# Kernel optimization log

Hardware: AMD Instinct MI355X
Metric: run time of the kernel (lower is better)

Reference implementation:

```python
import jax, jax.numpy as jnp
import numpy as np

TARGET_RADIUS = 0.95
EPS = 1e-8

def _spectral_norm_wh(W_h, u):
    # Power iteration (3 steps) is done under no_grad in the original torch code,
    # so u, v are constants w.r.t. differentiation.
    Ws = jax.lax.stop_gradient(W_h)
    v = None
    for _ in range(3):
        v = Ws.T @ u
        v = v / (jnp.linalg.norm(v) + EPS)
        u = Ws @ v
        u = u / (jnp.linalg.norm(u) + EPS)
    sigma = jnp.abs(u @ W_h @ v)  # gradient flows through W_h here
    return W_h * (TARGET_RADIUS / (sigma + EPS))


def setup_inputs() -> dict:
    key = jax.random.key(0)
    kx, kwx, kwh, ku = jax.random.split(key, 4)
    T, B, D = 2048, 8, 1024
    x = jax.random.normal(kx, (T, B, D), dtype=jnp.float32)
    h0 = jnp.zeros((B, D), dtype=jnp.float32)
    W_x = jax.random.normal(kwx, (D, D), dtype=jnp.float32) * 0.02
    W_h = jax.random.normal(kwh, (D, D), dtype=jnp.float32) * (1.0 / np.sqrt(D))
    b = jnp.zeros((D,), dtype=jnp.float32)
    u = jax.random.normal(ku, (D,), dtype=jnp.float32)
    u = u / jnp.linalg.norm(u)
    return {"x": x, "h0": h0, "W_x": W_x, "W_h": W_h, "b": b, "u": u}


def reference(x, h0, W_x, W_h, b, u):
    # x: [T, B, D], h0: [B, D]
    Wh = _spectral_norm_wh(W_h, u)
    # Input projection is independent of the recurrence: one big GEMM.
    pre = jnp.einsum('tbd,ed->tbe', x, W_x) + b  # [T, B, D]

    def step(h_prev, p_t):
        h_new = p_t + h_prev @ Wh.T  # linear recurrence, no tanh
        return h_new, h_new

    _, hs = jax.lax.scan(step, h0, pre)  # hs: [T, B, D]
    h_all = jnp.concatenate([h0[None], hs], axis=0)  # [T+1, B, D]
    output = hs * (hs * jax.nn.sigmoid(hs))  # h * silu(h)
    return output, h_all
```

## Files before the change

### kernel.cpp

```cpp
#include <hip/hip_runtime.h>
#include <hip/hip_bf16.h>

#define DEV __device__ __forceinline__

typedef __bf16 bf16x8 __attribute__((ext_vector_type(8)));
typedef float  f32x4  __attribute__((ext_vector_type(4)));
typedef unsigned short u16;

DEV u16   f2b(float f) { __bf16 h = (__bf16)f; return __builtin_bit_cast(u16, h); }
DEV float b2f(u16 x)   { return __builtin_bit_cast(float, ((unsigned)x) << 16); }

DEV void gl_lds16(const u16* g, u16* l) {
  __builtin_amdgcn_global_load_lds((const __attribute__((address_space(1))) void*)g,
                                   (__attribute__((address_space(3))) void*)l, 16, 0, 0);
}

DEV long arow(int m, int S, int j) {
  if (S > 0)  return ((long)((m >> 3) * S + j)) * 8 + (m & 7);
  if (S == 0) return m;
  return m & 7;
}

struct ZCfg {
  const u16 *A0, *A1, *A2, *A3, *A4;
  const u16 *B0, *B1, *B2, *B3, *B4;
  int S0, J0, S1, J1, S2, J2, S3, J3, S4, J4;
  int nseg, mvalid, q;
  const float* addc;
  const float* addf; int addS, addJ;
  const u16* addb; int abJ;
  float* outf;
  u16 *outb, *outbT, *outlo;
  u16* outm; int oS, oJ;
  float *hall, *out0;
};
struct GArgs { ZCfg z0, z1, z2, z3; };

template<int MODE>
__global__ __launch_bounds__(256) void gU(GArgs ga)
{
  ZCfg c;
  switch (blockIdx.z) { case 0: c = ga.z0; break; case 1: c = ga.z1; break;
                        case 2: c = ga.z2; break; default: c = ga.z3; break; }
  const int K = c.nseg << 10;

  int tid = threadIdx.x, lane = tid & 63, w = tid >> 6;
  int wrow = (w >> 1) << 5, wcol = (w & 1) << 5;
  int m0 = blockIdx.y << 6, e0 = blockIdx.x << 6;

  __shared__ u16 As[2][8192], Bs[2][8192];
  f32x4 acc[2][2] = {};

  int rA[4], cA[4];
#pragma unroll
  for (int j = 0; j < 4; ++j) {
    int p = (j * 4 + w) * 1024 + lane * 16;
    int r = p >> 8, o = (p & 255) ^ ((r & 7) << 4);
    rA[j] = r; cA[j] = o >> 1;
  }
  auto seg = [&](int i, const u16*& A, int& S, int& J, const u16*& B) {
    switch (i) {
      case 0: A = c.A0; S = c.S0; J = c.J0; B = c.B0; break;
      case 1: A = c.A1; S = c.S1; J = c.J1; B = c.B1; break;
      case 2: A = c.A2; S = c.S2; J = c.J2; B = c.B2; break;
      case 3: A = c.A3; S = c.S3; J = c.J3; B = c.B3; break;
      default: A = c.A4; S = c.S4; J = c.J4; B = c.B4; break;
    }
  };
  auto stage = [&](int buf, int kt) {
    int si = kt >> 10, kl = kt & 1023;
    const u16 *A, *B; int S, J;
    seg(si, A, S, J, B);
#pragma unroll
    for (int j = 0; j < 4; ++j) {
      int grow = m0 + rA[j];
      gl_lds16(A + arow(grow, S, J) * 1024 + kl + cA[j], &As[buf][(j * 4 + w) * 512]);
    }
#pragma unroll
    for (int j = 0; j < 4; ++j)
      gl_lds16(B + (size_t)(e0 + rA[j]) * 1024 + kl + cA[j], &Bs[buf][(j * 4 + w) * 512]);
  };

  stage(0, 0);
  asm volatile("s_waitcnt vmcnt(0)" ::: "memory");
  __syncthreads();

  int buf = 0;
  for (int kt = 0; kt < K; kt += 128, buf ^= 1) {
    if (kt + 128 < K) stage(buf ^ 1, kt + 128);
#pragma unroll
    for (int ks = 0; ks < 4; ++ks) {
      int oa = ks * 64 + ((lane >> 4) << 4);
      bf16x8 af[2], bf[2];
#pragma unroll
      for (int s = 0; s < 2; ++s) {
        int ra = wrow + s * 16 + (lane & 15);
        int rb = wcol + s * 16 + (lane & 15);
        af[s] = *(const bf16x8*)((const char*)&As[buf][0] + ra * 256 + (oa ^ ((ra & 7) << 4)));
        bf[s] = *(const bf16x8*)((const char*)&Bs[buf][0] + rb * 256 + (oa ^ ((rb & 7) << 4)));
      }
#pragma unroll
      for (int ms = 0; ms < 2; ++ms)
#pragma unroll
        for (int ns = 0; ns < 2; ++ns)
          acc[ms][ns] = __builtin_amdgcn_mfma_f32_16x16x32_bf16(af[ms], bf[ns], acc[ms][ns], 0, 0, 0);
    }
    asm volatile("s_waitcnt vmcnt(0)" ::: "memory");
    __syncthreads();
  }

  int l4 = ((lane >> 4) << 2), lc = lane & 15;
#pragma unroll
  for (int ms = 0; ms < 2; ++ms)
#pragma unroll
    for (int ns = 0; ns < 2; ++ns)
#pragma unroll
      for (int j = 0; j < 4; ++j) {
        int row = m0 + wrow + ms * 16 + l4 + j;
        int col = e0 + wcol + ns * 16 + lc;
        float v = acc[ms][ns][j];
        if (MODE == 0) {
          u16 h = f2b(v);
          if (c.outb)  c.outb[(size_t)row * 1024 + col] = h;
          if (c.outbT) c.outbT[(size_t)col * 1024 + row] = h;
        } else if (MODE == 1) {
          v += c.addc[col];
          c.outf[(size_t)row * 1024 + col] = v;
          c.outb[(size_t)row * 1024 + col] = f2b(v);
        } else if (MODE == 2) {
          if (c.addf) v += c.addf[arow(row, c.addS, c.addJ) * 1024 + col];
          if (row < c.mvalid) {
            if (c.outf) c.outf[(size_t)row * 1024 + col] = v;
            u16 hi = f2b(v);
            if (c.outb)  c.outb[(size_t)row * 1024 + col] = hi;
            if (c.outlo) c.outlo[(size_t)row * 1024 + col] = f2b(v - b2f(hi));
            if (c.outm)  c.outm[arow(row, c.oS, c.oJ) * 1024 + col] = hi;
          }
        } else {
          v += b2f(c.addb[arow(row, 4, c.abJ) * 1024 + col]);
          int t = (row >> 3) * 4 + c.q, b = row & 7;
          c.hall[(size_t)t * 8192 + b * 1024 + col] = v;
          float sg = 1.f / (1.f + __expf(-v));
          c.out0[(size_t)(t - 1) * 8192 + b * 1024 + col] = v * v * sg;
          if (c.outb) c.outb[(size_t)row * 1024 + col] = f2b(v);
        }
      }
}

__global__ void k_init(const float* __restrict__ u_in, const float* __restrict__ h0,
                       float* __restrict__ u_cur, float* __restrict__ v_acc,
                       float* __restrict__ u_acc, float* __restrict__ hall0)
{
  int i = blockIdx.x * 256 + threadIdx.x;
  if (i < 1024) { u_cur[i] = u_in[i]; v_acc[i] = 0.f; u_acc[i] = 0.f; }
  if (i < 8192) hall0[i] = h0[i];
}

__global__ void k_bnd0(const float* __restrict__ h0, float* __restrict__ bndS,
                       u16* __restrict__ bndSb, u16* __restrict__ bndSlo,
                       u16* __restrict__ bndb)
{
  int i = blockIdx.x * 256 + threadIdx.x;
  float h = h0[i];
  bndS[i] = h;
  u16 hi = f2b(h);
  bndSb[i] = hi;
  bndSlo[i] = f2b(h - b2f(hi));
  bndb[i] = hi;
}

__global__ void k_v(const float* __restrict__ W, const float* __restrict__ u_cur,
                    float* __restrict__ v_acc)
{
  int d = blockIdx.x * 256 + threadIdx.x;
  int e0 = blockIdx.y * 64;
  float a = 0.f;
  for (int e = e0; e < e0 + 64; ++e) a += W[(size_t)e * 1024 + d] * u_cur[e];
  atomicAdd(&v_acc[d], a);
}

__global__ void k_u(const float* __restrict__ W, const float* __restrict__ v_cur,
                    float* __restrict__ u_acc)
{
  int lg = threadIdx.x & 15, ei = threadIdx.x >> 4;
  int e = blockIdx.y * 16 + ei;
  int d0 = blockIdx.x * 512;
  float a = 0.f;
  for (int i = 0; i < 32; ++i) { int d = d0 + lg + 16 * i; a += W[(size_t)e * 1024 + d] * v_cur[d]; }
#pragma unroll
  for (int m = 1; m < 16; m <<= 1) a += __shfl_xor(a, m);
  if (lg == 0) atomicAdd(&u_acc[e], a);
}

__global__ void k_norm(const float* __restrict__ acc, float* __restrict__ outv,
                       float* __restrict__ z1)
{
  __shared__ float red[16];
  int t = threadIdx.x;
  float x = acc[t];
  float ss = x * x;
#pragma unroll
  for (int m = 1; m < 64; m <<= 1) ss += __shfl_xor(ss, m);
  if ((t & 63) == 0) red[t >> 6] = ss;
  __syncthreads();
  if (t < 64) {
    float s = (t < 16) ? red[t] : 0.f;
#pragma unroll
    for (int m = 1; m < 16; m <<= 1) s += __shfl_xor(s, m);
    if (t == 0) red[0] = s;
  }
  __syncthreads();
  float nrm = sqrtf(red[0]) + 1e-8f;
  outv[t] = x / nrm;
  z1[t] = 0.f;
}

__global__ void k_sigma(const float* __restrict__ acc, float* __restrict__ scale)
{
  __shared__ float red[16];
  int t = threadIdx.x;
  float x = acc[t];
  float ss = x * x;
#pragma unroll
  for (int m = 1; m < 64; m <<= 1) ss += __shfl_xor(ss, m);
  if ((t & 63) == 0) red[t >> 6] = ss;
  __syncthreads();
  if (t < 64) {
    float s = (t < 16) ? red[t] : 0.f;
#pragma unroll
    for (int m = 1; m < 16; m <<= 1) s += __shfl_xor(s, m);
    if (t == 0) {
      float sigma = s / (sqrtf(s) + 1e-8f);
      scale[0] = 0.95f / (sigma + 1e-8f);
    }
  }
}

__global__ void k_prep(const float* __restrict__ Wh, const float* __restrict__ Wx,
                       const float* __restrict__ scale, u16* __restrict__ wh_b,
                       u16* __restrict__ whT, u16* __restrict__ wxb)
{
  int i = blockIdx.x * 256 + threadIdx.x;
  float s = scale[0];
  int e = i >> 10, d = i & 1023;
  u16 hw = f2b(Wh[i] * s);
  wh_b[i] = hw;
  whT[(size_t)d * 1024 + e] = hw;
  wxb[i] = f2b(Wx[i]);
}

__global__ void k_cvt(const float* __restrict__ in, u16* __restrict__ out, int n)
{
  int i = (blockIdx.x * 256 + threadIdx.x) * 4;
  if (i >= n) return;
  float4 v = *(const float4*)(in + i);
  ushort4 o;
  o.x = f2b(v.x); o.y = f2b(v.y); o.z = f2b(v.z); o.w = f2b(v.w);
  *(ushort4*)(out + i) = o;
}

__global__ void k_gather(const float* __restrict__ lC, u16* __restrict__ lamH,
                         u16* __restrict__ lamL)
{
  int i = blockIdx.x * 256 + threadIdx.x;
  int r = i >> 8, e4 = (i & 255) * 4;
  int src = (r >> 3) * 128 + (r & 7);
  float4 v = *(const float4*)(lC + (size_t)src * 1024 + e4);
  ushort4 hi, lo;
  hi.x = f2b(v.x); lo.x = f2b(v.x - b2f(hi.x));
  hi.y = f2b(v.y); lo.y = f2b(v.y - b2f(hi.y));
  hi.z = f2b(v.z); lo.z = f2b(v.z - b2f(hi.z));
  hi.w = f2b(v.w); lo.w = f2b(v.w - b2f(hi.w));
  *(ushort4*)(lamH + (size_t)r * 1024 + e4) = hi;
  *(ushort4*)(lamL + (size_t)r * 1024 + e4) = lo;
}

static void setseg(ZCfg& z, int i, const u16* A, int S, int J, const u16* B) {
  switch (i) {
    case 0: z.A0 = A; z.S0 = S; z.J0 = J; z.B0 = B; break;
    case 1: z.A1 = A; z.S1 = S; z.J1 = J; z.B1 = B; break;
    case 2: z.A2 = A; z.S2 = S; z.J2 = J; z.B2 = B; break;
    case 3: z.A3 = A; z.S3 = S; z.J3 = J; z.B3 = B; break;
    default: z.A4 = A; z.S4 = S; z.J4 = J; z.B4 = B; break;
  }
}

extern "C" void kernel_launch(void* const* d_in, const int* in_sizes, int n_in,
                              void* d_out, int out_size, void* d_ws, size_t ws_size,
                              hipStream_t stream)
{
  (void)in_sizes; (void)n_in; (void)out_size; (void)ws_size;
  const float* x  = (const float*)d_in[0];
  const float* h0 = (const float*)d_in[1];
  const float* Wx = (const float*)d_in[2];
  const float* Wh = (const float*)d_in[3];
  const float* bv = (const float*)d_in[4];
  const float* uv = (const float*)d_in[5];

  float* out0 = (float*)d_out;
  float* hall = out0 + 16777216;

  const size_t M1 = 1048576;
  char* ws = (char*)d_ws;
  u16*   pre_b = (u16*)(ws);
  u16*   wh_b  = (u16*)(ws + 32 * M1);
  u16*   bnd_b = (u16*)(ws + 34 * M1);
  u16*   lb0   = (u16*)(ws + 42 * M1);
  float* u_cur = (float*)(ws + 50 * M1);
  float* v_cur = u_cur + 1024;
  float* v_acc = u_cur + 2048;
  float* u_acc = u_cur + 3072;
  float* scale = u_cur + 4096;

  float* preF = out0;

  char* HBS = (char*)hall + 32768;
  u16*   xb   = (u16*)(HBS);
  float* lC   = (float*)(HBS);
  u16*   lCb  = (u16*)(HBS + 16 * M1);
  float* lamF = (float*)(HBS + 24 * M1);
  u16* lamH0  = (u16*)(HBS + 25 * M1);
  u16* lamH1  = (u16*)(HBS + 25 * M1 + 524288);
  u16* lamL0  = (u16*)(HBS + 26 * M1);
  u16* lamL1  = (u16*)(HBS + 26 * M1 + 524288);
  float* bndS = (float*)(HBS + 27 * M1);
  u16* bndSb  = (u16*)(HBS + 28 * M1);
  u16* bndSlo = (u16*)(HBS + 28 * M1 + 524288);
  u16* pcH0   = (u16*)(HBS + 29 * M1);
  u16* pcH1   = (u16*)(HBS + 29 * M1 + 524288);
  u16* pcL0   = (u16*)(HBS + 30 * M1);
  u16* pcL1   = (u16*)(HBS + 30 * M1 + 524288);
  auto slot = [&](int k) { return (u16*)(HBS + 32 * M1 + (size_t)k * 2 * M1); };
  u16* whT  = slot(0);
  u16* wxb  = slot(1);
  u16* W2   = slot(2);
  u16* W2T  = slot(3);
  u16* W3   = slot(4);
  u16* W4   = slot(5);
  u16* W4T  = slot(6);
  u16* W8   = slot(7);
  u16* W8T  = slot(8);
  u16* W12  = slot(9);
  u16* W16  = slot(10);
  u16* W16T = slot(11);
  u16* W32  = slot(12);
  u16* W32T = slot(13);
  u16* W64  = slot(14);
  u16* W64T = slot(15);
  u16* W128 = W8T, *W128T = W16T, *W192 = whT, *W256 = wxb;

  k_init<<<32, 256, 0, stream>>>(uv, h0, u_cur, v_acc, u_acc, hall);

  for (int it = 0; it < 3; ++it) {
    k_v<<<dim3(4, 16), 256, 0, stream>>>(Wh, u_cur, v_acc);
    k_norm<<<1, 1024, 0, stream>>>(v_acc, v_cur, u_acc);
    k_u<<<dim3(2, 64), 256, 0, stream>>>(Wh, v_cur, u_acc);
    if (it < 2) k_norm<<<1, 1024, 0, stream>>>(u_acc, u_cur, v_acc);
    else        k_sigma<<<1, 1024, 0, stream>>>(u_acc, scale);
  }
  k_prep<<<4096, 256, 0, stream>>>(Wh, Wx, scale, wh_b, whT, wxb);
  k_cvt<<<16384, 256, 0, stream>>>(x, xb, 16777216);

  { GArgs a{}; ZCfg& z = a.z0;
    setseg(z, 0, xb, 0, 0, wxb);
    z.nseg = 1; z.addc = bv; z.outf = preF; z.outb = pre_b;
    gU<1><<<dim3(16, 256, 1), 256, 0, stream>>>(a); }

  auto sqz = [](ZCfg& z, const u16* A, const u16* B, u16* o, u16* oT) {
    z.A0 = A; z.S0 = 0; z.J0 = 0; z.B0 = B; z.nseg = 1; z.outb = o; z.outbT = oT;
  };
  { GArgs a{}; sqz(a.z0, wh_b, whT, W2, W2T);
    gU<0><<<dim3(16, 16, 1), 256, 0, stream>>>(a); }
  { GArgs a{}; sqz(a.z0, W2, whT, W3, nullptr); sqz(a.z1, W2, W2T, W4, W4T);
    gU<0><<<dim3(16, 16, 2), 256, 0, stream>>>(a); }
  { GArgs a{}; sqz(a.z0, W4, W4T, W8, W8T);
    gU<0><<<dim3(16, 16, 1), 256, 0, stream>>>(a); }
  { GArgs a{}; sqz(a.z0, W8, W4T, W12, nullptr); sqz(a.z1, W8, W8T, W16, W16T);
    gU<0><<<dim3(16, 16, 2), 256, 0, stream>>>(a); }
  { GArgs a{}; sqz(a.z0, W16, W16T, W32, W32T);
    gU<0><<<dim3(16, 16, 1), 256, 0, stream>>>(a); }
  { GArgs a{}; sqz(a.z0, W32, W32T, W64, W64T);
    gU<0><<<dim3(16, 16, 1), 256, 0, stream>>>(a); }
  { GArgs a{}; sqz(a.z0, W64, W64T, W128, W128T);
    gU<0><<<dim3(16, 16, 1), 256, 0, stream>>>(a); }
  { GArgs a{}; sqz(a.z0, W128, W64T, W192, nullptr); sqz(a.z1, W128, W128T, W256, nullptr);
    gU<0><<<dim3(16, 16, 2), 256, 0, stream>>>(a); }

  { GArgs a{}; ZCfg& z = a.z0;
    setseg(z, 0, pre_b, 4, 0, W3);
    setseg(z, 1, pre_b, 4, 1, W2);
    setseg(z, 2, pre_b, 4, 2, wh_b);
    z.nseg = 3; z.mvalid = 4096;
    z.addf = preF; z.addS = 4; z.addJ = 3;
    z.outf = lC; z.outb = lCb;
    gU<2><<<dim3(16, 64, 1), 256, 0, stream>>>(a); }

  k_bnd0<<<32, 256, 0, stream>>>(h0, bndS, bndSb, bndSlo, bnd_b);

  k_gather<<<256, 256, 0, stream>>>(lC, lamH0, lamL0);
  {
    const u16 *chH = lamH0, *chL = lamL0;
    int j0s[3] = {1, 5, 9};
    int pp = 1;
    for (int i = 0; i < 3; ++i) {
      u16* nxH = pp ? lamH1 : lamH0;
      u16* nxL = pp ? lamL1 : lamL0;
      GArgs a{}; ZCfg& z = a.z0;
      setseg(z, 0, chH, 0, 0, W16); setseg(z, 1, chL, 0, 0, W16);
      setseg(z, 2, lCb, 16, j0s[i],     W12);
      setseg(z, 3, lCb, 16, j0s[i] + 1, W8);
      setseg(z, 4, lCb, 16, j0s[i] + 2, W4);
      z.nseg = 5; z.mvalid = 256;
      z.addf = lC; z.addS = 16; z.addJ = j0s[i] + 3;
      z.outb = nxH; z.outlo = nxL;
      gU<2><<<dim3(16, 4, 1), 256, 0, stream>>>(a);
      chH = nxH; chL = nxL; pp ^= 1;
    }
    GArgs a{}; ZCfg& z = a.z0;
    setseg(z, 0, chH, 0, 0, W12); setseg(z, 1, chL, 0, 0, W12);
    setseg(z, 2, lCb, 16, 13, W8); setseg(z, 3, lCb, 16, 14, W4);
    z.nseg = 4; z.mvalid = 256;
    z.addf = lC; z.addS = 16; z.addJ = 15;
    z.outf = lamF; z.outb = lamH0; z.outlo = lamL0;
    gU<2><<<dim3(16, 4, 1), 256, 0, stream>>>(a);
  }

  {
    const u16* w64s[4] = { W64, W128, W192, W256 };
    for (int sb2 = 0; sb2 < 32; sb2 += 4) {
      int zmax = (sb2 == 28) ? 3 : 4;
      GArgs a{};
      ZCfg* zs[4] = { &a.z0, &a.z1, &a.z2, &a.z3 };
      for (int zz = 1; zz <= zmax; ++zz) {
        ZCfg& z = *zs[zz - 1];
        setseg(z, 0, bndSb + (size_t)sb2 * 8192, -1, 0, w64s[zz - 1]);
        int ns = 1;
        for (int i = 0; i < zz - 1; ++i)
          setseg(z, ns++, lamH0 + (size_t)(sb2 + i) * 8192, -1, 0, w64s[zz - 2 - i]);
        z.nseg = ns; z.mvalid = 8;
        z.addf = lamF + (size_t)(sb2 + zz - 1) * 8192; z.addS = -1;
        z.outb = bndSb + (size_t)(sb2 + zz) * 8192;
        z.outlo = bndSlo + (size_t)(sb2 + zz) * 8192;
        z.outm = bnd_b + (size_t)16 * (sb2 + zz) * 8192; z.oS = 0;
      }
      gU<2><<<dim3(16, 1, zmax), 256, 0, stream>>>(a);
    }
  }

  {
    const u16* w4s[4] = { W4, W8, W12, W16 };
    const u16* cinH[4] = { bndSb, pcH0, pcH1, pcH0 };
    const u16* cinL[4] = { bndSlo, pcL0, pcL1, pcL0 };
    u16* coutH[4] = { pcH0, pcH1, pcH0, nullptr };
    u16* coutL[4] = { pcL0, pcL1, pcL0, nullptr };
    for (int t4 = 0; t4 < 4; ++t4) {
      int jb = 4 * t4;
      int zmax = (t4 == 3) ? 3 : 4;
      GArgs a{};
      ZCfg* zs[4] = { &a.z0, &a.z1, &a.z2, &a.z3 };
      for (int zz = 1; zz <= zmax; ++zz) {
        ZCfg& z = *zs[zz - 1];
        setseg(z, 0, cinH[t4], 0, 0, w4s[zz - 1]);
        setseg(z, 1, cinL[t4], 0, 0, w4s[zz - 1]);
        int ns = 2;
        for (int i = 0; i < zz - 1; ++i)
          setseg(z, ns++, lCb, 16, jb + i, w4s[zz - 2 - i]);
        z.nseg = ns; z.mvalid = 256;
        z.addf = lC; z.addS = 16; z.addJ = jb + zz - 1;
        z.outm = bnd_b; z.oS = 16; z.oJ = jb + zz;
        if (zz == 4) { z.outb = coutH[t4]; z.outlo = coutL[t4]; }
      }
      gU<2><<<dim3(16, 4, zmax), 256, 0, stream>>>(a);
    }
  }

  {
    const u16* ins[4]  = { bnd_b, lb0, bnd_b, lb0 };
    u16*       outs[4] = { lb0, bnd_b, lb0, nullptr };
    for (int q = 1; q <= 4; ++q) {
      GArgs a{}; ZCfg& z = a.z0;
      setseg(z, 0, ins[q - 1], 0, 0, wh_b);
      z.nseg = 1; z.q = q;
      z.addb = pre_b; z.abJ = q - 1;
      z.hall = hall; z.out0 = out0;
      z.outb = outs[q - 1];
      gU<3><<<dim3(16, 64, 1), 256, 0, stream>>>(a);
    }
  }
}
```

Before: 1.095 ms.

## Co-schedule matrix-power squarings with recurrence GEMMs and drop fp32 pre buffer

The GEMM kernel now takes its mode at runtime, so matrix-power squaring GEMMs can share a launch via blockIdx.z with the input projection, the chunk-scan GEMMs and the lambda chain. This cuts launch count and fills idle CUs in the small-grid launches. It also removes the fp32 pre-activation buffer and adds the bf16 pre instead, folds k_bnd0 into k_init, and writes the lambda gather directly from the GEMM epilogue. A grouped block index remap is added for L2 locality. The price is runtime mode branching, early-exit blocks in the padded grids, and somewhat lower precision from the bf16 pre-add.

```diff
diff --git a/kernel.cpp b/kernel.cpp
--- a/kernel.cpp
+++ b/kernel.cpp
@@ -25,28 +25,35 @@
   const u16 *A0, *A1, *A2, *A3, *A4;
   const u16 *B0, *B1, *B2, *B3, *B4;
   int S0, J0, S1, J1, S2, J2, S3, J3, S4, J4;
-  int nseg, mvalid, q;
+  int nseg, mvalid, q, mode, ylim;
   const float* addc;
-  const float* addf; int addS, addJ;
-  const u16* addb; int abJ;
+  const float* addf;
+  const u16*   addb; int addS, addJ;
   float* outf;
   u16 *outb, *outbT, *outlo;
   u16* outm; int oS, oJ;
+  u16 *glamH, *glamL;
   float *hall, *out0;
 };
 struct GArgs { ZCfg z0, z1, z2, z3; };
 
-template<int MODE>
 __global__ __launch_bounds__(256) void gU(GArgs ga)
 {
   ZCfg c;
   switch (blockIdx.z) { case 0: c = ga.z0; break; case 1: c = ga.z1; break;
                         case 2: c = ga.z2; break; default: c = ga.z3; break; }
+
+  int gx = gridDim.x;
+  int fid = blockIdx.y * gx + blockIdx.x;
+  int nwg = gx * gridDim.y;
+  int idx = (fid & 7) * (nwg >> 3) + (fid >> 3);
+  int mt = idx / gx, et = idx % gx;
+  if (mt >= c.ylim) return;
+  int m0 = mt << 6, e0 = et << 6;
+
   const int K = c.nseg << 10;
-
   int tid = threadIdx.x, lane = tid & 63, w = tid >> 6;
   int wrow = (w >> 1) << 5, wcol = (w & 1) << 5;
-  int m0 = blockIdx.y << 6, e0 = blockIdx.x << 6;
 
   __shared__ u16 As[2][8192], Bs[2][8192];
   f32x4 acc[2][2] = {};
@@ -119,25 +126,28 @@
         int row = m0 + wrow + ms * 16 + l4 + j;
         int col = e0 + wcol + ns * 16 + lc;
         float v = acc[ms][ns][j];
-        if (MODE == 0) {
+        if (c.mode == 0) {
           u16 h = f2b(v);
           if (c.outb)  c.outb[(size_t)row * 1024 + col] = h;
           if (c.outbT) c.outbT[(size_t)col * 1024 + row] = h;
-        } else if (MODE == 1) {
-          v += c.addc[col];
-          c.outf[(size_t)row * 1024 + col] = v;
-          c.outb[(size_t)row * 1024 + col] = f2b(v);
-        } else if (MODE == 2) {
-          if (c.addf) v += c.addf[arow(row, c.addS, c.addJ) * 1024 + col];
+        } else if (c.mode == 2) {
+          if (c.addc) v += c.addc[col];
+          if (c.addb)      v += b2f(c.addb[arow(row, c.addS, c.addJ) * 1024 + col]);
+          else if (c.addf) v += c.addf[arow(row, c.addS, c.addJ) * 1024 + col];
           if (row < c.mvalid) {
             if (c.outf) c.outf[(size_t)row * 1024 + col] = v;
             u16 hi = f2b(v);
             if (c.outb)  c.outb[(size_t)row * 1024 + col] = hi;
             if (c.outlo) c.outlo[(size_t)row * 1024 + col] = f2b(v - b2f(hi));
             if (c.outm)  c.outm[arow(row, c.oS, c.oJ) * 1024 + col] = hi;
+            if (c.glamH && ((row >> 3) & 15) == 0) {
+              int r2 = ((row >> 3) >> 4) * 8 + (row & 7);
+              c.glamH[(size_t)r2 * 1024 + col] = hi;
+              c.glamL[(size_t)r2 * 1024 + col] = f2b(v - b2f(hi));
+            }
           }
         } else {
-          v += b2f(c.addb[arow(row, 4, c.abJ) * 1024 + col]);
+          v += b2f(c.addb[arow(row, c.addS, c.addJ) * 1024 + col]);
           int t = (row >> 3) * 4 + c.q, b = row & 7;
           c.hall[(size_t)t * 8192 + b * 1024 + col] = v;
           float sg = 1.f / (1.f + __expf(-v));
@@ -149,24 +159,20 @@
 
 __global__ void k_init(const float* __restrict__ u_in, const float* __restrict__ h0,
                        float* __restrict__ u_cur, float* __restrict__ v_acc,
-                       float* __restrict__ u_acc, float* __restrict__ hall0)
+                       float* __restrict__ u_acc, float* __restrict__ hall0,
+                       u16* __restrict__ bndSb, u16* __restrict__ bndSlo,
+                       u16* __restrict__ bndb)
 {
   int i = blockIdx.x * 256 + threadIdx.x;
   if (i < 1024) { u_cur[i] = u_in[i]; v_acc[i] = 0.f; u_acc[i] = 0.f; }
-  if (i < 8192) hall0[i] = h0[i];
-}
-
-__global__ void k_bnd0(const float* __restrict__ h0, float* __restrict__ bndS,
-                       u16* __restrict__ bndSb, u16* __restrict__ bndSlo,
-                       u16* __restrict__ bndb)
-{
-  int i = blockIdx.x * 256 + threadIdx.x;
-  float h = h0[i];
-  bndS[i] = h;
-  u16 hi = f2b(h);
-  bndSb[i] = hi;
-  bndSlo[i] = f2b(h - b2f(hi));
-  bndb[i] = hi;
+  if (i < 8192) {
+    float h = h0[i];
+    hall0[i] = h;
+    u16 hi = f2b(h);
+    bndSb[i] = hi;
+    bndSlo[i] = f2b(h - b2f(hi));
+    bndb[i] = hi;
+  }
 }
 
 __global__ void k_v(const float* __restrict__ W, const float* __restrict__ u_cur,
@@ -259,22 +265,6 @@
   *(ushort4*)(out + i) = o;
 }
 
-__global__ void k_gather(const float* __restrict__ lC, u16* __restrict__ lamH,
-                         u16* __restrict__ lamL)
-{
-  int i = blockIdx.x * 256 + threadIdx.x;
-  int r = i >> 8, e4 = (i & 255) * 4;
-  int src = (r >> 3) * 128 + (r & 7);
-  float4 v = *(const float4*)(lC + (size_t)src * 1024 + e4);
-  ushort4 hi, lo;
-  hi.x = f2b(v.x); lo.x = f2b(v.x - b2f(hi.x));
-  hi.y = f2b(v.y); lo.y = f2b(v.y - b2f(hi.y));
-  hi.z = f2b(v.z); lo.z = f2b(v.z - b2f(hi.z));
-  hi.w = f2b(v.w); lo.w = f2b(v.w - b2f(hi.w));
-  *(ushort4*)(lamH + (size_t)r * 1024 + e4) = hi;
-  *(ushort4*)(lamL + (size_t)r * 1024 + e4) = lo;
-}
-
 static void setseg(ZCfg& z, int i, const u16* A, int S, int J, const u16* B) {
   switch (i) {
     case 0: z.A0 = A; z.S0 = S; z.J0 = J; z.B0 = B; break;
@@ -284,6 +274,10 @@
     default: z.A4 = A; z.S4 = S; z.J4 = J; z.B4 = B; break;
   }
 }
+static void setsq(ZCfg& z, const u16* A, const u16* B, u16* o, u16* oT) {
+  z.A0 = A; z.S0 = 0; z.J0 = 0; z.B0 = B; z.nseg = 1;
+  z.outb = o; z.outbT = oT; z.mode = 0; z.ylim = 16;
+}
 
 extern "C" void kernel_launch(void* const* d_in, const int* in_sizes, int n_in,
                               void* d_out, int out_size, void* d_ws, size_t ws_size,
@@ -306,13 +300,13 @@
   u16*   wh_b  = (u16*)(ws + 32 * M1);
   u16*   bnd_b = (u16*)(ws + 34 * M1);
   u16*   lb0   = (u16*)(ws + 42 * M1);
-  float* u_cur = (float*)(ws + 50 * M1);
+  u16*   bndSb = (u16*)(ws + 50 * M1);
+  u16*   bndSlo= (u16*)(ws + 50 * M1 + 524288);
+  float* u_cur = (float*)(ws + 51 * M1);
   float* v_cur = u_cur + 1024;
   float* v_acc = u_cur + 2048;
   float* u_acc = u_cur + 3072;
   float* scale = u_cur + 4096;
-
-  float* preF = out0;
 
   char* HBS = (char*)hall + 32768;
   u16*   xb   = (u16*)(HBS);
@@ -323,13 +317,10 @@
   u16* lamH1  = (u16*)(HBS + 25 * M1 + 524288);
   u16* lamL0  = (u16*)(HBS + 26 * M1);
   u16* lamL1  = (u16*)(HBS + 26 * M1 + 524288);
-  float* bndS = (float*)(HBS + 27 * M1);
-  u16* bndSb  = (u16*)(HBS + 28 * M1);
-  u16* bndSlo = (u16*)(HBS + 28 * M1 + 524288);
-  u16* pcH0   = (u16*)(HBS + 29 * M1);
-  u16* pcH1   = (u16*)(HBS + 29 * M1 + 524288);
-  u16* pcL0   = (u16*)(HBS + 30 * M1);
-  u16* pcL1   = (u16*)(HBS + 30 * M1 + 524288);
+  u16* pcH0   = (u16*)(HBS + 27 * M1);
+  u16* pcH1   = (u16*)(HBS + 27 * M1 + 524288);
+  u16* pcL0   = (u16*)(HBS + 28 * M1);
+  u16* pcL1   = (u16*)(HBS + 28 * M1 + 524288);
   auto slot = [&](int k) { return (u16*)(HBS + 32 * M1 + (size_t)k * 2 * M1); };
   u16* whT  = slot(0);
   u16* wxb  = slot(1);
@@ -349,7 +340,8 @@
   u16* W64T = slot(15);
   u16* W128 = W8T, *W128T = W16T, *W192 = whT, *W256 = wxb;
 
-  k_init<<<32, 256, 0, stream>>>(uv, h0, u_cur, v_acc, u_acc, hall);
+  k_init<<<32, 256, 0, stream>>>(uv, h0, u_cur, v_acc, u_acc, hall,
+                                 bndSb, bndSlo, bnd_b);
 
   for (int it = 0; it < 3; ++it) {
     k_v<<<dim3(4, 16), 256, 0, stream>>>(Wh, u_cur, v_acc);
@@ -363,66 +355,59 @@
 
   { GArgs a{}; ZCfg& z = a.z0;
     setseg(z, 0, xb, 0, 0, wxb);
-    z.nseg = 1; z.addc = bv; z.outf = preF; z.outb = pre_b;
-    gU<1><<<dim3(16, 256, 1), 256, 0, stream>>>(a); }
-
-  auto sqz = [](ZCfg& z, const u16* A, const u16* B, u16* o, u16* oT) {
-    z.A0 = A; z.S0 = 0; z.J0 = 0; z.B0 = B; z.nseg = 1; z.outb = o; z.outbT = oT;
-  };
-  { GArgs a{}; sqz(a.z0, wh_b, whT, W2, W2T);
-    gU<0><<<dim3(16, 16, 1), 256, 0, stream>>>(a); }
-  { GArgs a{}; sqz(a.z0, W2, whT, W3, nullptr); sqz(a.z1, W2, W2T, W4, W4T);
-    gU<0><<<dim3(16, 16, 2), 256, 0, stream>>>(a); }
-  { GArgs a{}; sqz(a.z0, W4, W4T, W8, W8T);
-    gU<0><<<dim3(16, 16, 1), 256, 0, stream>>>(a); }
-  { GArgs a{}; sqz(a.z0, W8, W4T, W12, nullptr); sqz(a.z1, W8, W8T, W16, W16T);
-    gU<0><<<dim3(16, 16, 2), 256, 0, stream>>>(a); }
-  { GArgs a{}; sqz(a.z0, W16, W16T, W32, W32T);
-    gU<0><<<dim3(16, 16, 1), 256, 0, stream>>>(a); }
-  { GArgs a{}; sqz(a.z0, W32, W32T, W64, W64T);
-    gU<0><<<dim3(16, 16, 1), 256, 0, stream>>>(a); }
-  { GArgs a{}; sqz(a.z0, W64, W64T, W128, W128T);
-    gU<0><<<dim3(16, 16, 1), 256, 0, stream>>>(a); }
-  { GArgs a{}; sqz(a.z0, W128, W64T, W192, nullptr); sqz(a.z1, W128, W128T, W256, nullptr);
-    gU<0><<<dim3(16, 16, 2), 256, 0, stream>>>(a); }
+    z.nseg = 1; z.mode = 2; z.ylim = 256; z.mvalid = 16384;
+    z.addc = bv; z.outb = pre_b;
+    setsq(a.z1, wh_b, whT, W2, W2T);
+    gU<<<dim3(16, 256, 2), 256, 0, stream>>>(a); }
+
+  { GArgs a{}; setsq(a.z0, W2, whT, W3, nullptr); setsq(a.z1, W2, W2T, W4, W4T);
+    gU<<<dim3(16, 16, 2), 256, 0, stream>>>(a); }
 
   { GArgs a{}; ZCfg& z = a.z0;
     setseg(z, 0, pre_b, 4, 0, W3);
     setseg(z, 1, pre_b, 4, 1, W2);
     setseg(z, 2, pre_b, 4, 2, wh_b);
-    z.nseg = 3; z.mvalid = 4096;
-    z.addf = preF; z.addS = 4; z.addJ = 3;
+    z.nseg = 3; z.mode = 2; z.ylim = 64; z.mvalid = 4096;
+    z.addb = pre_b; z.addS = 4; z.addJ = 3;
     z.outf = lC; z.outb = lCb;
-    gU<2><<<dim3(16, 64, 1), 256, 0, stream>>>(a); }
-
-  k_bnd0<<<32, 256, 0, stream>>>(h0, bndS, bndSb, bndSlo, bnd_b);
-
-  k_gather<<<256, 256, 0, stream>>>(lC, lamH0, lamL0);
+    z.glamH = lamH0; z.glamL = lamL0;
+    setsq(a.z1, W4, W4T, W8, W8T);
+    gU<<<dim3(16, 64, 2), 256, 0, stream>>>(a); }
+
+  { GArgs a{}; setsq(a.z0, W8, W4T, W12, nullptr); setsq(a.z1, W8, W8T, W16, W16T);
+    gU<<<dim3(16, 16, 2), 256, 0, stream>>>(a); }
+
   {
     const u16 *chH = lamH0, *chL = lamL0;
     int j0s[3] = {1, 5, 9};
-    int pp = 1;
+    u16* nxH[3] = { lamH1, lamH0, lamH1 };
+    u16* nxL[3] = { lamL1, lamL0, lamL1 };
+    const u16* sqA[3] = { W16, W32, W64 };
+    const u16* sqB[3] = { W16T, W32T, W64T };
+    u16* sqO[3] = { W32, W64, W128 };
+    u16* sqT[3] = { W32T, W64T, W128T };
     for (int i = 0; i < 3; ++i) {
-      u16* nxH = pp ? lamH1 : lamH0;
-      u16* nxL = pp ? lamL1 : lamL0;
       GArgs a{}; ZCfg& z = a.z0;
       setseg(z, 0, chH, 0, 0, W16); setseg(z, 1, chL, 0, 0, W16);
       setseg(z, 2, lCb, 16, j0s[i],     W12);
       setseg(z, 3, lCb, 16, j0s[i] + 1, W8);
       setseg(z, 4, lCb, 16, j0s[i] + 2, W4);
-      z.nseg = 5; z.mvalid = 256;
+      z.nseg = 5; z.mode = 2; z.ylim = 4; z.mvalid = 256;
       z.addf = lC; z.addS = 16; z.addJ = j0s[i] + 3;
-      z.outb = nxH; z.outlo = nxL;
-      gU<2><<<dim3(16, 4, 1), 256, 0, stream>>>(a);
-      chH = nxH; chL = nxL; pp ^= 1;
+      z.outb = nxH[i]; z.outlo = nxL[i];
+      setsq(a.z1, sqA[i], sqB[i], sqO[i], sqT[i]);
+      gU<<<dim3(16, 16, 2), 256, 0, stream>>>(a);
+      chH = nxH[i]; chL = nxL[i];
     }
     GArgs a{}; ZCfg& z = a.z0;
     setseg(z, 0, chH, 0, 0, W12); setseg(z, 1, chL, 0, 0, W12);
     setseg(z, 2, lCb, 16, 13, W8); setseg(z, 3, lCb, 16, 14, W4);
-    z.nseg = 4; z.mvalid = 256;
+    z.nseg = 4; z.mode = 2; z.ylim = 4; z.mvalid = 256;
     z.addf = lC; z.addS = 16; z.addJ = 15;
     z.outf = lamF; z.outb = lamH0; z.outlo = lamL0;
-    gU<2><<<dim3(16, 4, 1), 256, 0, stream>>>(a);
+    setsq(a.z1, W128, W64T, W192, nullptr);
+    setsq(a.z2, W128, W128T, W256, nullptr);
+    gU<<<dim3(16, 16, 3), 256, 0, stream>>>(a);
   }
 
   {
@@ -437,13 +422,13 @@
         int ns = 1;
         for (int i = 0; i < zz - 1; ++i)
           setseg(z, ns++, lamH0 + (size_t)(sb2 + i) * 8192, -1, 0, w64s[zz - 2 - i]);
-        z.nseg = ns; z.mvalid = 8;
+        z.nseg = ns; z.mode = 2; z.ylim = 1; z.mvalid = 8;
         z.addf = lamF + (size_t)(sb2 + zz - 1) * 8192; z.addS = -1;
         z.outb = bndSb + (size_t)(sb2 + zz) * 8192;
         z.outlo = bndSlo + (size_t)(sb2 + zz) * 8192;
         z.outm = bnd_b + (size_t)16 * (sb2 + zz) * 8192; z.oS = 0;
       }
-      gU<2><<<dim3(16, 1, zmax), 256, 0, stream>>>(a);
+      gU<<<dim3(16, 1, zmax), 256, 0, stream>>>(a);
     }
   }
 
@@ -465,12 +450,12 @@
         int ns = 2;
         for (int i = 0; i < zz - 1; ++i)
           setseg(z, ns++, lCb, 16, jb + i, w4s[zz - 2 - i]);
-        z.nseg = ns; z.mvalid = 256;
+        z.nseg = ns; z.mode = 2; z.ylim = 4; z.mvalid = 256;
         z.addf = lC; z.addS = 16; z.addJ = jb + zz - 1;
         z.outm = bnd_b; z.oS = 16; z.oJ = jb + zz;
         if (zz == 4) { z.outb = coutH[t4]; z.outlo = coutL[t4]; }
       }
-      gU<2><<<dim3(16, 4, zmax), 256, 0, stream>>>(a);
+      gU<<<dim3(16, 4, zmax), 256, 0, stream>>>(a);
     }
   }
 
@@ -480,11 +465,11 @@
     for (int q = 1; q <= 4; ++q) {
       GArgs a{}; ZCfg& z = a.z0;
       setseg(z, 0, ins[q - 1], 0, 0, wh_b);
-      z.nseg = 1; z.q = q;
-      z.addb = pre_b; z.abJ = q - 1;
+      z.nseg = 1; z.mode = 3; z.ylim = 64; z.q = q;
+      z.addb = pre_b; z.addS = 4; z.addJ = q - 1;
       z.hall = hall; z.out0 = out0;
       z.outb = outs[q - 1];
-      gU<3><<<dim3(16, 64, 1), 256, 0, stream>>>(a);
-    }
-  }
-}
+      gU<<<dim3(16, 64, 1), 256, 0, stream>>>(a);
+    }
+  }
+}
```

Result: slower. 1.144 ms (+4.5%).
